# Optimization experiments

Measured on AMD Instinct MI355X. Metric: run time of the kernel, lower is better.

## Reference

```python
import jax, jax.numpy as jnp
import numpy as np
from jax import lax

DN = ('NCHW', 'OIHW', 'NCHW')


def squash(x):
    # x: [..., d]; squared-norm over last dim
    sq = jnp.sum(x * x, axis=-1, keepdims=True)
    return sq * x / ((1.0 + sq) * jnp.sqrt(sq))


def setup_inputs() -> dict:
    key = jax.random.key(0)
    ks = jax.random.split(key, 6)
    B = 512
    x = jax.random.normal(ks[0], (B, 1, 28, 28), dtype=jnp.float32)
    conv1_w = jax.random.normal(ks[1], (256, 1, 9, 9), dtype=jnp.float32) * 0.05
    conv1_b = jnp.zeros((256,), dtype=jnp.float32)
    conv2_w = jax.random.normal(ks[2], (256, 256, 9, 9), dtype=jnp.float32) * 0.02
    conv2_b = jnp.zeros((256,), dtype=jnp.float32)
    # W: [num_routes=1152, num_capsules=10, out_channels=16, in_channels=8]
    W = jax.random.normal(ks[3], (1152, 10, 16, 8), dtype=jnp.float32)
    return {"x": x, "conv1_w": conv1_w, "conv1_b": conv1_b,
            "conv2_w": conv2_w, "conv2_b": conv2_b, "W": W}


def reference(x, conv1_w, conv1_b, conv2_w, conv2_b, W):
    B = x.shape[0]
    # conv1 + ReLU: [B,1,28,28] -> [B,256,20,20]
    h = lax.conv_general_dilated(x, conv1_w, (1, 1), 'VALID', dimension_numbers=DN)
    h = jax.nn.relu(h + conv1_b[None, :, None, None])
    # primary capsule conv: [B,256,20,20] -> [B,256,6,6], stride 2
    h = lax.conv_general_dilated(h, conv2_w, (2, 2), 'VALID', dimension_numbers=DN)
    h = h + conv2_b[None, :, None, None]
    # reshape to capsules [B, 1152, 8] (matches torch .view on NCHW) and squash
    u = squash(h.reshape(B, -1, 8))
    # u_hat[b,r,c,o] = W[r,c,o,i] @ u[b,r,i]
    u_hat = jnp.einsum('rcoi,bri->brco', W, u)  # [B,1152,10,16]
    R, C = W.shape[0], W.shape[1]
    b_ij = jnp.zeros((R, C), dtype=x.dtype)
    num_iterations = 3
    for it in range(num_iterations):
        c_ij = jax.nn.softmax(b_ij, axis=0)          # softmax over routes
        s_j = jnp.einsum('rc,brco->bco', c_ij, u_hat)  # [B,10,16]
        v_j = squash(s_j)
        if it < num_iterations - 1:
            a_ij = jnp.einsum('brco,bco->brc', u_hat, v_j)  # agreement
            b_ij = b_ij + a_ij.mean(axis=0)
    return v_j  # [B,10,16]
```

## Files before the change

kernel.cpp:

```cpp
#include <hip/hip_runtime.h>
#include <stdint.h>


typedef unsigned short u16;
typedef unsigned int u32;
typedef short short8 __attribute__((ext_vector_type(8)));
typedef float f32x4 __attribute__((ext_vector_type(4)));

__device__ __forceinline__ u16 f2bf(float f) {
  u32 u = __float_as_uint(f);
  return (u16)((u + 0x7FFFu + ((u >> 16) & 1u)) >> 16);
}

__device__ __forceinline__ void gload_lds16(const void* g, void* l) {
  __builtin_amdgcn_global_load_lds(
      (const __attribute__((address_space(1))) void*)g,
      (__attribute__((address_space(3))) void*)l, 16, 0, 0);
}

__global__ __launch_bounds__(256) void conv1_kernel(
    const float* __restrict__ x, const float* __restrict__ w1,
    const float* __restrict__ b1, u16* __restrict__ hT) {
  int b = blockIdx.x;
  int co0 = blockIdx.y * 128;
  int t = threadIdx.x;
  if (t >= 200) return;
  int oh = t / 10, ow0 = (t % 10) * 2;
  const float* xb = x + (size_t)b * 784;
  float patch[9][10];
#pragma unroll
  for (int kh = 0; kh < 9; ++kh)
#pragma unroll
    for (int j = 0; j < 10; ++j) patch[kh][j] = xb[(oh + kh) * 28 + ow0 + j];
  u16* hb = hT + ((size_t)b * 400 + oh * 20 + ow0) * 256 + co0;
  for (int c8 = 0; c8 < 16; ++c8) {
    u16 o0[8], o1[8];
#pragma unroll
    for (int cc = 0; cc < 8; ++cc) {
      int co = co0 + c8 * 8 + cc;
      const float* wc = w1 + co * 81;
      float a0 = 0.f, a1 = 0.f;
#pragma unroll
      for (int kh = 0; kh < 9; ++kh)
#pragma unroll
        for (int kw = 0; kw < 9; ++kw) {
          float wv = wc[kh * 9 + kw];
          a0 = fmaf(wv, patch[kh][kw], a0);
          a1 = fmaf(wv, patch[kh][kw + 1], a1);
        }
      float bias = b1[co];
      o0[cc] = f2bf(fmaxf(a0 + bias, 0.f));
      o1[cc] = f2bf(fmaxf(a1 + bias, 0.f));
    }
    *(uint4*)(hb + c8 * 8) = *(uint4*)o0;
    *(uint4*)(hb + 256 + c8 * 8) = *(uint4*)o1;
  }
}

__global__ __launch_bounds__(256) void prep_w2_kernel(
    const float* __restrict__ w2, u16* __restrict__ A2) {
  int idx = blockIdx.x * 256 + threadIdx.x;
  int co = idx / 20736, k = idx - co * 20736;
  int t = k >> 8, ci = k & 255;
  A2[idx] = f2bf(w2[(size_t)(co * 256 + ci) * 81 + t]);
}

__global__ __launch_bounds__(256) void init_u_kernel(
    const float* __restrict__ b2, float* __restrict__ u) {
  int i = blockIdx.x * 256 + threadIdx.x;
  int b = i / 2304, j0 = (i - b * 2304) * 4;
  float4 v;
  v.x = b2[j0 / 36]; v.y = b2[(j0 + 1) / 36];
  v.z = b2[(j0 + 2) / 36]; v.w = b2[(j0 + 3) / 36];
  *(float4*)(u + (size_t)b * 9216 + j0) = v;
}

__global__ __launch_bounds__(256) void conv2_kernel(
    const u16* __restrict__ hT, const u16* __restrict__ A2,
    float* __restrict__ u) {
  __shared__ __align__(16) u16 Al[2][128 * 64];
  __shared__ __align__(16) u16 Bl[2][128 * 64];
  int bx = blockIdx.x;
  int mb = bx & 1, kz = (bx >> 1) & 3, nbk = bx >> 3;
  int m0 = mb * 128, n0 = nbk * 128;
  int t_begin = (81 * kz) >> 2, t_end = (81 * (kz + 1)) >> 2;
  int NS = (t_end - t_begin) * 4;
  int tid = threadIdx.x;
  int lane = tid & 63, wave = tid >> 6;
  int wr = wave >> 1, wc = wave & 1;

  int srow8 = lane >> 3;
  int q = lane & 7;
  int rowbase = wave * 32 + srow8;
  int qs = q ^ srow8;
  size_t A_off[4];
  int B_off[4];
#pragma unroll
  for (int j = 0; j < 4; ++j) {
    int row = rowbase + j * 8;
    A_off[j] = (size_t)(m0 + row) * 20736 + qs * 8;
    int n = n0 + row;
    int nb_ = n / 36;
    int sp = n - nb_ * 36;
    int oh = sp / 6, ow = sp - oh * 6;
    B_off[j] = ((nb_ * 20 + 2 * oh) * 20 + 2 * ow) * 256 + qs * 8;
  }
  int ldsbase = wave * 4096;

  int fr = lane & 15, fg = lane >> 4;
  int rs = fr & 7;
  int arow[4], bcol[4];
#pragma unroll
  for (int m = 0; m < 4; ++m) {
    arow[m] = (wr * 64 + m * 16 + fr) * 128;
    bcol[m] = (wc * 64 + m * 16 + fr) * 128;
  }
  int xg0 = ((0 + fg) ^ rs) << 4;
  int xg1 = ((4 + fg) ^ rs) << 4;

  f32x4 acc[4][4] = {};

  auto STAGE = [&](int s, int buf) {
    int t = t_begin + (s >> 2);
    int kk = s & 3;
    int kh = t / 9, kw = t - kh * 9;
    int toffA = t * 256 + kk * 64;
    int toffB = (kh * 20 + kw) * 256 + kk * 64;
#pragma unroll
    for (int j = 0; j < 4; ++j) {
      gload_lds16(A2 + A_off[j] + toffA, (char*)Al[buf] + ldsbase + j * 1024);
      gload_lds16(hT + B_off[j] + toffB, (char*)Bl[buf] + ldsbase + j * 1024);
    }
  };

  STAGE(0, 0);
  __syncthreads();
  int cur = 0;
  for (int s = 0; s < NS; ++s) {
    if (s + 1 < NS) STAGE(s + 1, cur ^ 1);
    const char* Ab = (const char*)Al[cur];
    const char* Bb = (const char*)Bl[cur];
    short8 af[4], bf_[4];
#pragma unroll
    for (int m = 0; m < 4; ++m) af[m] = *(const short8*)(Ab + arow[m] + xg0);
#pragma unroll
    for (int nn = 0; nn < 4; ++nn) bf_[nn] = *(const short8*)(Bb + bcol[nn] + xg0);
#pragma unroll
    for (int m = 0; m < 4; ++m)
#pragma unroll
      for (int nn = 0; nn < 4; ++nn)
        acc[m][nn] = __builtin_amdgcn_mfma_f32_16x16x32_bf16(
            af[m], bf_[nn], acc[m][nn], 0, 0, 0);
#pragma unroll
    for (int m = 0; m < 4; ++m) af[m] = *(const short8*)(Ab + arow[m] + xg1);
#pragma unroll
    for (int nn = 0; nn < 4; ++nn) bf_[nn] = *(const short8*)(Bb + bcol[nn] + xg1);
#pragma unroll
    for (int m = 0; m < 4; ++m)
#pragma unroll
      for (int nn = 0; nn < 4; ++nn)
        acc[m][nn] = __builtin_amdgcn_mfma_f32_16x16x32_bf16(
            af[m], bf_[nn], acc[m][nn], 0, 0, 0);
    __syncthreads();
    cur ^= 1;
  }
#pragma unroll
  for (int nn = 0; nn < 4; ++nn) {
    int cn = n0 + wc * 64 + nn * 16 + fr;
    int ob = cn / 36;
    int os = cn - ob * 36;
    float* op = u + (size_t)ob * 9216 + os;
#pragma unroll
    for (int m = 0; m < 4; ++m) {
      int row0 = m0 + wr * 64 + m * 16 + fg * 4;
#pragma unroll
      for (int qq = 0; qq < 4; ++qq)
        atomicAdd(op + (row0 + qq) * 36, acc[m][nn][qq]);
    }
  }
}

__global__ __launch_bounds__(256) void squash_kernel(
    const float* __restrict__ u, u16* __restrict__ ub, u16* __restrict__ ubT) {
  int idx = blockIdx.x * 256 + threadIdx.x;
  int r = idx >> 9, b = idx & 511;
  const float* up = u + (size_t)b * 9216 + r * 8;
  float4 a = *(const float4*)up;
  float4 c = *(const float4*)(up + 4);
  float sq = a.x * a.x + a.y * a.y + a.z * a.z + a.w * a.w +
             c.x * c.x + c.y * c.y + c.z * c.z + c.w * c.w;
  float f = sqrtf(sq) / (1.0f + sq);
  u16 o[8];
  o[0] = f2bf(a.x * f); o[1] = f2bf(a.y * f);
  o[2] = f2bf(a.z * f); o[3] = f2bf(a.w * f);
  o[4] = f2bf(c.x * f); o[5] = f2bf(c.y * f);
  o[6] = f2bf(c.z * f); o[7] = f2bf(c.w * f);
  *(uint4*)(ub + ((size_t)b * 1152 + r) * 8) = *(uint4*)o;
#pragma unroll
  for (int i = 0; i < 8; ++i) ubT[(size_t)(r * 8 + i) * 512 + b] = o[i];
}

__global__ __launch_bounds__(256) void softmax_c_kernel(
    const float* __restrict__ bij, float* __restrict__ cT) {
  int c = blockIdx.x;
  int tid = threadIdx.x;
  __shared__ float red[256];
  float mx = -1e30f;
  for (int r = tid; r < 1152; r += 256) mx = fmaxf(mx, bij[r * 10 + c]);
  red[tid] = mx;
  __syncthreads();
  for (int s = 128; s > 0; s >>= 1) {
    if (tid < s) red[tid] = fmaxf(red[tid], red[tid + s]);
    __syncthreads();
  }
  mx = red[0];
  __syncthreads();
  float sum = 0.f;
  for (int r = tid; r < 1152; r += 256) sum += expf(bij[r * 10 + c] - mx);
  red[tid] = sum;
  __syncthreads();
  for (int s = 128; s > 0; s >>= 1) {
    if (tid < s) red[tid] += red[tid + s];
    __syncthreads();
  }
  float inv = 1.0f / red[0];
  for (int r = tid; r < 1152; r += 256)
    cT[c * 1152 + r] = expf(bij[r * 10 + c] - mx) * inv;
}

__global__ __launch_bounds__(256) void gemm_s_kernel(
    const float* __restrict__ W, const float* __restrict__ cT,
    const u16* __restrict__ ub, float* __restrict__ s) {
  __shared__ __align__(16) u16 Asl[160 * 72];
  __shared__ __align__(16) u16 Bsl[64 * 72];
  int nb = blockIdx.x & 7, kzi = blockIdx.x >> 3;
  int n0 = nb * 64, k0 = kzi * 128;
  int tid = threadIdx.x;
  int lane = tid & 63, wave = tid >> 6;
  int fr = lane & 15, fg = lane >> 4;
  f32x4 acc[10] = {};
#pragma unroll
  for (int st = 0; st < 2; ++st) {
    int kb = k0 + st * 64;
    __syncthreads();
#pragma unroll
    for (int j = 0; j < 5; ++j) {
      int c5 = tid + j * 256;
      int row = c5 >> 3, qq = c5 & 7;
      int cls = row >> 4, o = row & 15;
      int r = (kb + qq * 8) >> 3;
      const float* wp = W + (size_t)r * 1280 + cls * 128 + o * 8;
      float4 w0 = *(const float4*)wp;
      float4 w1 = *(const float4*)(wp + 4);
      float cs = cT[cls * 1152 + r];
      u16 ov[8];
      ov[0] = f2bf(w0.x * cs); ov[1] = f2bf(w0.y * cs);
      ov[2] = f2bf(w0.z * cs); ov[3] = f2bf(w0.w * cs);
      ov[4] = f2bf(w1.x * cs); ov[5] = f2bf(w1.y * cs);
      ov[6] = f2bf(w1.z * cs); ov[7] = f2bf(w1.w * cs);
      *(uint4*)((char*)Asl + row * 144 + qq * 16) = *(uint4*)ov;
    }
#pragma unroll
    for (int j = 0; j < 2; ++j) {
      int c2 = tid + j * 256;
      int row = c2 >> 3, qq = c2 & 7;
      *(uint4*)((char*)Bsl + row * 144 + qq * 16) =
          *(const uint4*)(ub + (size_t)(n0 + row) * 9216 + kb + qq * 8);
    }
    __syncthreads();
#pragma unroll
    for (int s2 = 0; s2 < 2; ++s2) {
      int xg = (s2 * 4 + fg) * 16;
      short8 bf0 = *(const short8*)((char*)Bsl + (wave * 16 + fr) * 144 + xg);
#pragma unroll
      for (int m = 0; m < 10; ++m) {
        short8 af = *(const short8*)((char*)Asl + (m * 16 + fr) * 144 + xg);
        acc[m] = __builtin_amdgcn_mfma_f32_16x16x32_bf16(af, bf0, acc[m], 0, 0, 0);
      }
    }
  }
  int bcol = n0 + wave * 16 + fr;
#pragma unroll
  for (int m = 0; m < 10; ++m)
#pragma unroll
    for (int qq = 0; qq < 4; ++qq)
      atomicAdd(s + (m * 16 + fg * 4 + qq) * 512 + bcol, acc[m][qq]);
}

__global__ __launch_bounds__(256) void squash_v_kernel(
    float* __restrict__ s, u16* __restrict__ vb,
    float* __restrict__ outp, int write_out) {
  int idx = blockIdx.x * 256 + threadIdx.x;
  int c = idx >> 9, b = idx & 511;
  float vals[16];
  float sq = 0.f;
#pragma unroll
  for (int o = 0; o < 16; ++o) {
    float v = s[(c * 16 + o) * 512 + b];
    vals[o] = v;
    sq += v * v;
  }
#pragma unroll
  for (int o = 0; o < 16; ++o) s[(c * 16 + o) * 512 + b] = 0.f;
  float f = sqrtf(sq) / (1.0f + sq);
  if (write_out) {
#pragma unroll
    for (int o = 0; o < 16; ++o) outp[((size_t)b * 10 + c) * 16 + o] = vals[o] * f;
  } else {
#pragma unroll
    for (int o = 0; o < 16; ++o) vb[(c * 16 + o) * 512 + b] = f2bf(vals[o] * f);
  }
}

__global__ __launch_bounds__(256) void gemm_gc_kernel(
    const u16* __restrict__ vb, const u16* __restrict__ ubT,
    const float* __restrict__ W, float* __restrict__ bij) {
  __shared__ __align__(16) u16 Agl[160 * 72];
  __shared__ __align__(16) u16 Bgl[128 * 72];
  __shared__ float Gl[160 * 129];
  int nb = blockIdx.x % 72, kzi = blockIdx.x / 72;
  int n0 = nb * 128, k0 = kzi * 256;
  int tid = threadIdx.x;
  int lane = tid & 63, wave = tid >> 6;
  int fr = lane & 15, fg = lane >> 4;
  f32x4 acc[10][2] = {};
  for (int st = 0; st < 4; ++st) {
    int kb = k0 + st * 64;
    __syncthreads();
#pragma unroll
    for (int j = 0; j < 5; ++j) {
      int c5 = tid + j * 256;
      int row = c5 >> 3, qq = c5 & 7;
      *(uint4*)((char*)Agl + row * 144 + qq * 16) =
          *(const uint4*)(vb + (size_t)row * 512 + kb + qq * 8);
    }
#pragma unroll
    for (int j = 0; j < 4; ++j) {
      int c4 = tid + j * 256;
      int row = c4 >> 3, qq = c4 & 7;
      *(uint4*)((char*)Bgl + row * 144 + qq * 16) =
          *(const uint4*)(ubT + (size_t)(n0 + row) * 512 + kb + qq * 8);
    }
    __syncthreads();
#pragma unroll
    for (int s2 = 0; s2 < 2; ++s2) {
      int xg = (s2 * 4 + fg) * 16;
      short8 bfv[2];
#pragma unroll
      for (int nn = 0; nn < 2; ++nn)
        bfv[nn] = *(const short8*)((char*)Bgl + (wave * 32 + nn * 16 + fr) * 144 + xg);
#pragma unroll
      for (int m = 0; m < 10; ++m) {
        short8 af = *(const short8*)((char*)Agl + (m * 16 + fr) * 144 + xg);
#pragma unroll
        for (int nn = 0; nn < 2; ++nn)
          acc[m][nn] = __builtin_amdgcn_mfma_f32_16x16x32_bf16(af, bfv[nn],
                                                              acc[m][nn], 0, 0, 0);
      }
    }
  }
#pragma unroll
  for (int m = 0; m < 10; ++m)
#pragma unroll
    for (int nn = 0; nn < 2; ++nn) {
      int col = wave * 32 + nn * 16 + fr;
#pragma unroll
      for (int qq = 0; qq < 4; ++qq)
        Gl[(m * 16 + fg * 4 + qq) * 129 + col] = acc[m][nn][qq];
    }
  __syncthreads();
  if (tid < 160) {
    int rl = tid / 10, c = tid - rl * 10;
    int r = (n0 >> 3) + rl;
    const float* wp = W + (size_t)r * 1280 + c * 128;
    float a = 0.f;
#pragma unroll 4
    for (int o = 0; o < 16; ++o) {
      const float* gp = &Gl[(c * 16 + o) * 129 + rl * 8];
#pragma unroll
      for (int i = 0; i < 8; ++i) a = fmaf(wp[o * 8 + i], gp[i], a);
    }
    atomicAdd(&bij[r * 10 + c], a * (1.0f / 512.0f));
  }
}

extern "C" void kernel_launch(void* const* d_in, const int* in_sizes, int n_in,
                              void* d_out, int out_size, void* d_ws, size_t ws_size,
                              hipStream_t stream) {
  const float* x  = (const float*)d_in[0];
  const float* w1 = (const float*)d_in[1];
  const float* b1 = (const float*)d_in[2];
  const float* w2 = (const float*)d_in[3];
  const float* b2 = (const float*)d_in[4];
  const float* W  = (const float*)d_in[5];
  char* ws = (char*)d_ws;
  u16*   hT  = (u16*)ws;
  u16*   A2  = (u16*)(ws + 104857600);
  float* u   = (float*)(ws + 115474432);
  float* bij = (float*)(ws + 134348800);
  float* cT  = (float*)(ws + 134394880);
  float* s   = (float*)(ws + 134440960);
  u16*   ub  = (u16*)ws;
  u16*   ubT = (u16*)(ws + 9437184);
  u16*   vb  = (u16*)(ws + 21823488);
  float* out = (float*)d_out;

  hipMemsetAsync(bij, 0, 46080, stream);
  hipMemsetAsync(s, 0, 327680, stream);
  init_u_kernel<<<4608, 256, 0, stream>>>(b2, u);
  conv1_kernel<<<dim3(512, 2), 256, 0, stream>>>(x, w1, b1, hT);
  prep_w2_kernel<<<20736, 256, 0, stream>>>(w2, A2);
  conv2_kernel<<<1152, 256, 0, stream>>>(hT, A2, u);
  squash_kernel<<<2304, 256, 0, stream>>>(u, ub, ubT);
  for (int it = 0; it < 3; ++it) {
    softmax_c_kernel<<<10, 256, 0, stream>>>(bij, cT);
    gemm_s_kernel<<<576, 256, 0, stream>>>(W, cT, ub, s);
    squash_v_kernel<<<20, 256, 0, stream>>>(s, vb, out, it == 2 ? 1 : 0);
    if (it < 2) gemm_gc_kernel<<<144, 256, 0, stream>>>(vb, ubT, W, bij);
  }
}
```

Before: 736.0 us.

## Retile conv2 with 4-stage LDS pipeline and fuse softmax into routing GEMM

Conv2 becomes a 512-thread block covering all 256 output channels by 256 columns, with split-K of 8. It stages 32-wide K slices through a 4-deep LDS ring using vmcnt waits and a single barrier per step, aiming to hide global-to-LDS latency and reuse operands better. The separate softmax kernel is removed: each gemm_s block recomputes the per-class max and sum over b_ij and applies exp inline, which saves a launch at the cost of redundant reduction work. The split-K factors of gemm_s and gemm_gc are also rebalanced. The larger accumulator set raises register pressure.

```diff
diff --git a/kernel.cpp b/kernel.cpp
--- a/kernel.cpp
+++ b/kernel.cpp
@@ -75,95 +75,76 @@
   *(float4*)(u + (size_t)b * 9216 + j0) = v;
 }
 
-__global__ __launch_bounds__(256) void conv2_kernel(
+__global__ __launch_bounds__(512) void conv2_kernel(
     const u16* __restrict__ hT, const u16* __restrict__ A2,
     float* __restrict__ u) {
-  __shared__ __align__(16) u16 Al[2][128 * 64];
-  __shared__ __align__(16) u16 Bl[2][128 * 64];
+  __shared__ __align__(16) u16 lds[4 * 16384];
   int bx = blockIdx.x;
-  int mb = bx & 1, kz = (bx >> 1) & 3, nbk = bx >> 3;
-  int m0 = mb * 128, n0 = nbk * 128;
-  int t_begin = (81 * kz) >> 2, t_end = (81 * (kz + 1)) >> 2;
-  int NS = (t_end - t_begin) * 4;
+  int nbk = bx >> 3, kz = bx & 7;
+  int n0 = nbk * 256;
+  int tb = (81 * kz) >> 3, te = (81 * (kz + 1)) >> 3;
+  int NS = (te - tb) * 8;
   int tid = threadIdx.x;
-  int lane = tid & 63, wave = tid >> 6;
-  int wr = wave >> 1, wc = wave & 1;
-
-  int srow8 = lane >> 3;
-  int q = lane & 7;
-  int rowbase = wave * 32 + srow8;
-  int qs = q ^ srow8;
-  size_t A_off[4];
-  int B_off[4];
-#pragma unroll
-  for (int j = 0; j < 4; ++j) {
-    int row = rowbase + j * 8;
-    A_off[j] = (size_t)(m0 + row) * 20736 + qs * 8;
-    int n = n0 + row;
-    int nb_ = n / 36;
-    int sp = n - nb_ * 36;
-    int oh = sp / 6, ow = sp - oh * 6;
-    B_off[j] = ((nb_ * 20 + 2 * oh) * 20 + 2 * ow) * 256 + qs * 8;
-  }
-  int ldsbase = wave * 4096;
-
+  int lane = tid & 63, w = tid >> 6;
+  int wr = w >> 2, wc = w & 3;
   int fr = lane & 15, fg = lane >> 4;
-  int rs = fr & 7;
-  int arow[4], bcol[4];
-#pragma unroll
-  for (int m = 0; m < 4; ++m) {
-    arow[m] = (wr * 64 + m * 16 + fr) * 128;
-    bcol[m] = (wc * 64 + m * 16 + fr) * 128;
-  }
-  int xg0 = ((0 + fg) ^ rs) << 4;
-  int xg1 = ((4 + fg) ^ rs) << 4;
-
-  f32x4 acc[4][4] = {};
-
-  auto STAGE = [&](int s, int buf) {
-    int t = t_begin + (s >> 2);
-    int kk = s & 3;
+
+  int CA0 = w * 128 + lane, CA1 = CA0 + 64;
+  int r0 = CA0 >> 2, r1 = CA1 >> 2;
+  int q0 = ((CA0 & 3) ^ (r0 & 3)) << 3;
+  int q1 = ((CA1 & 3) ^ (r1 & 3)) << 3;
+  int Aoff0 = r0 * 20736 + q0;
+  int Aoff1 = r1 * 20736 + q1;
+  int Boff0, Boff1;
+  {
+    int n = n0 + r0; int b = n / 36, sp = n - b * 36, oh = sp / 6, ow = sp - oh * 6;
+    Boff0 = (b * 400 + oh * 40 + ow * 2) * 256 + q0;
+    n = n0 + r1; b = n / 36; sp = n - b * 36; oh = sp / 6; ow = sp - oh * 6;
+    Boff1 = (b * 400 + oh * 40 + ow * 2) * 256 + q1;
+  }
+
+  auto STAGE = [&](int s) {
+    int buf = s & 3;
+    int t = tb + (s >> 3), sub = s & 7;
     int kh = t / 9, kw = t - kh * 9;
-    int toffA = t * 256 + kk * 64;
-    int toffB = (kh * 20 + kw) * 256 + kk * 64;
-#pragma unroll
-    for (int j = 0; j < 4; ++j) {
-      gload_lds16(A2 + A_off[j] + toffA, (char*)Al[buf] + ldsbase + j * 1024);
-      gload_lds16(hT + B_off[j] + toffB, (char*)Bl[buf] + ldsbase + j * 1024);
-    }
+    int ao = t * 256 + sub * 32;
+    int bo = (kh * 20 + kw) * 256 + sub * 32;
+    char* base = (char*)lds + buf * 32768 + w * 2048;
+    gload_lds16(A2 + Aoff0 + ao, base);
+    gload_lds16(A2 + Aoff1 + ao, base + 1024);
+    gload_lds16(hT + Boff0 + bo, base + 16384);
+    gload_lds16(hT + Boff1 + bo, base + 17408);
   };
 
-  STAGE(0, 0);
-  __syncthreads();
-  int cur = 0;
+  int coff = (fg ^ (fr & 3)) << 4;
+  int abase[8], bbase[4];
+#pragma unroll
+  for (int m = 0; m < 8; ++m) abase[m] = (wr * 128 + m * 16 + fr) * 64 + coff;
+#pragma unroll
+  for (int n = 0; n < 4; ++n) bbase[n] = 16384 + (wc * 64 + n * 16 + fr) * 64 + coff;
+
+  f32x4 acc[8][4] = {};
+
+  STAGE(0); STAGE(1); STAGE(2);
   for (int s = 0; s < NS; ++s) {
-    if (s + 1 < NS) STAGE(s + 1, cur ^ 1);
-    const char* Ab = (const char*)Al[cur];
-    const char* Bb = (const char*)Bl[cur];
-    short8 af[4], bf_[4];
-#pragma unroll
-    for (int m = 0; m < 4; ++m) af[m] = *(const short8*)(Ab + arow[m] + xg0);
-#pragma unroll
-    for (int nn = 0; nn < 4; ++nn) bf_[nn] = *(const short8*)(Bb + bcol[nn] + xg0);
-#pragma unroll
-    for (int m = 0; m < 4; ++m)
-#pragma unroll
-      for (int nn = 0; nn < 4; ++nn)
-        acc[m][nn] = __builtin_amdgcn_mfma_f32_16x16x32_bf16(
-            af[m], bf_[nn], acc[m][nn], 0, 0, 0);
-#pragma unroll
-    for (int m = 0; m < 4; ++m) af[m] = *(const short8*)(Ab + arow[m] + xg1);
-#pragma unroll
-    for (int nn = 0; nn < 4; ++nn) bf_[nn] = *(const short8*)(Bb + bcol[nn] + xg1);
-#pragma unroll
-    for (int m = 0; m < 4; ++m)
-#pragma unroll
-      for (int nn = 0; nn < 4; ++nn)
-        acc[m][nn] = __builtin_amdgcn_mfma_f32_16x16x32_bf16(
-            af[m], bf_[nn], acc[m][nn], 0, 0, 0);
-    __syncthreads();
-    cur ^= 1;
-  }
+    asm volatile("s_waitcnt vmcnt(8)" ::: "memory");
+    __builtin_amdgcn_s_barrier();
+    asm volatile("" ::: "memory");
+    if (s + 3 < NS) STAGE(s + 3);
+    const char* bb = (const char*)lds + (s & 3) * 32768;
+    short8 af[8], bv[4];
+#pragma unroll
+    for (int m = 0; m < 8; ++m) af[m] = *(const short8*)(bb + abase[m]);
+#pragma unroll
+    for (int n = 0; n < 4; ++n) bv[n] = *(const short8*)(bb + bbase[n]);
+#pragma unroll
+    for (int m = 0; m < 8; ++m)
+#pragma unroll
+      for (int n = 0; n < 4; ++n)
+        acc[m][n] = __builtin_amdgcn_mfma_f32_16x16x32_bf16(af[m], bv[n],
+                                                            acc[m][n], 0, 0, 0);
+  }
+
 #pragma unroll
   for (int nn = 0; nn < 4; ++nn) {
     int cn = n0 + wc * 64 + nn * 16 + fr;
@@ -171,8 +152,8 @@
     int os = cn - ob * 36;
     float* op = u + (size_t)ob * 9216 + os;
 #pragma unroll
-    for (int m = 0; m < 4; ++m) {
-      int row0 = m0 + wr * 64 + m * 16 + fg * 4;
+    for (int m = 0; m < 8; ++m) {
+      int row0 = wr * 128 + m * 16 + fg * 4;
 #pragma unroll
       for (int qq = 0; qq < 4; ++qq)
         atomicAdd(op + (row0 + qq) * 36, acc[m][nn][qq]);
@@ -200,47 +181,33 @@
   for (int i = 0; i < 8; ++i) ubT[(size_t)(r * 8 + i) * 512 + b] = o[i];
 }
 
-__global__ __launch_bounds__(256) void softmax_c_kernel(
-    const float* __restrict__ bij, float* __restrict__ cT) {
-  int c = blockIdx.x;
-  int tid = threadIdx.x;
-  __shared__ float red[256];
-  float mx = -1e30f;
-  for (int r = tid; r < 1152; r += 256) mx = fmaxf(mx, bij[r * 10 + c]);
-  red[tid] = mx;
-  __syncthreads();
-  for (int s = 128; s > 0; s >>= 1) {
-    if (tid < s) red[tid] = fmaxf(red[tid], red[tid + s]);
-    __syncthreads();
-  }
-  mx = red[0];
-  __syncthreads();
-  float sum = 0.f;
-  for (int r = tid; r < 1152; r += 256) sum += expf(bij[r * 10 + c] - mx);
-  red[tid] = sum;
-  __syncthreads();
-  for (int s = 128; s > 0; s >>= 1) {
-    if (tid < s) red[tid] += red[tid + s];
-    __syncthreads();
-  }
-  float inv = 1.0f / red[0];
-  for (int r = tid; r < 1152; r += 256)
-    cT[c * 1152 + r] = expf(bij[r * 10 + c] - mx) * inv;
-}
-
 __global__ __launch_bounds__(256) void gemm_s_kernel(
-    const float* __restrict__ W, const float* __restrict__ cT,
+    const float* __restrict__ W, const float* __restrict__ bij,
     const u16* __restrict__ ub, float* __restrict__ s) {
   __shared__ __align__(16) u16 Asl[160 * 72];
   __shared__ __align__(16) u16 Bsl[64 * 72];
+  __shared__ float smx[10], sinv[10];
   int nb = blockIdx.x & 7, kzi = blockIdx.x >> 3;
-  int n0 = nb * 64, k0 = kzi * 128;
+  int n0 = nb * 64, k0 = kzi * 256;
   int tid = threadIdx.x;
   int lane = tid & 63, wave = tid >> 6;
   int fr = lane & 15, fg = lane >> 4;
+
+  for (int c = wave; c < 10; c += 4) {
+    float mx = -1e30f;
+    for (int r = lane; r < 1152; r += 64) mx = fmaxf(mx, bij[r * 10 + c]);
+#pragma unroll
+    for (int d = 1; d < 64; d <<= 1) mx = fmaxf(mx, __shfl_xor(mx, d, 64));
+    float sm = 0.f;
+    for (int r = lane; r < 1152; r += 64) sm += expf(bij[r * 10 + c] - mx);
+#pragma unroll
+    for (int d = 1; d < 64; d <<= 1) sm += __shfl_xor(sm, d, 64);
+    if (lane == 0) { smx[c] = mx; sinv[c] = 1.0f / sm; }
+  }
+
   f32x4 acc[10] = {};
 #pragma unroll
-  for (int st = 0; st < 2; ++st) {
+  for (int st = 0; st < 4; ++st) {
     int kb = k0 + st * 64;
     __syncthreads();
 #pragma unroll
@@ -252,7 +219,7 @@
       const float* wp = W + (size_t)r * 1280 + cls * 128 + o * 8;
       float4 w0 = *(const float4*)wp;
       float4 w1 = *(const float4*)(wp + 4);
-      float cs = cT[cls * 1152 + r];
+      float cs = expf(bij[r * 10 + cls] - smx[cls]) * sinv[cls];
       u16 ov[8];
       ov[0] = f2bf(w0.x * cs); ov[1] = f2bf(w0.y * cs);
       ov[2] = f2bf(w0.z * cs); ov[3] = f2bf(w0.w * cs);
@@ -319,12 +286,13 @@
   __shared__ __align__(16) u16 Bgl[128 * 72];
   __shared__ float Gl[160 * 129];
   int nb = blockIdx.x % 72, kzi = blockIdx.x / 72;
-  int n0 = nb * 128, k0 = kzi * 256;
+  int n0 = nb * 128, k0 = kzi * 128;
   int tid = threadIdx.x;
   int lane = tid & 63, wave = tid >> 6;
   int fr = lane & 15, fg = lane >> 4;
   f32x4 acc[10][2] = {};
-  for (int st = 0; st < 4; ++st) {
+#pragma unroll
+  for (int st = 0; st < 2; ++st) {
     int kb = k0 + st * 64;
     __syncthreads();
 #pragma unroll
@@ -398,7 +366,6 @@
   u16*   A2  = (u16*)(ws + 104857600);
   float* u   = (float*)(ws + 115474432);
   float* bij = (float*)(ws + 134348800);
-  float* cT  = (float*)(ws + 134394880);
   float* s   = (float*)(ws + 134440960);
   u16*   ub  = (u16*)ws;
   u16*   ubT = (u16*)(ws + 9437184);
@@ -410,12 +377,11 @@
   init_u_kernel<<<4608, 256, 0, stream>>>(b2, u);
   conv1_kernel<<<dim3(512, 2), 256, 0, stream>>>(x, w1, b1, hT);
   prep_w2_kernel<<<20736, 256, 0, stream>>>(w2, A2);
-  conv2_kernel<<<1152, 256, 0, stream>>>(hT, A2, u);
+  conv2_kernel<<<576, 512, 0, stream>>>(hT, A2, u);
   squash_kernel<<<2304, 256, 0, stream>>>(u, ub, ubT);
   for (int it = 0; it < 3; ++it) {
-    softmax_c_kernel<<<10, 256, 0, stream>>>(bij, cT);
-    gemm_s_kernel<<<576, 256, 0, stream>>>(W, cT, ub, s);
+    gemm_s_kernel<<<288, 256, 0, stream>>>(W, bij, ub, s);
     squash_v_kernel<<<20, 256, 0, stream>>>(s, vb, out, it == 2 ? 1 : 0);
-    if (it < 2) gemm_gc_kernel<<<144, 256, 0, stream>>>(vb, ubT, W, bij);
-  }
-}
+    if (it < 2) gemm_gc_kernel<<<288, 256, 0, stream>>>(vb, ubT, W, bij);
+  }
+}
```

New measurement: 791.0 us. 7.5% more time.
